# Kernel tuning notes

Hardware: AMD Instinct MI355X
Metric: run time of the kernel (lower is better)

## Reference

```python
import jax, jax.numpy as jnp
import numpy as np

N = 30000   # fluid particles
E = 480000  # edges
F = 4       # fluidFeatures (in channels)
P = 8       # RBF basis size per dim (dims=[8], 1D)
LAYERS = [32, 64, 64, 2]


def hat_basis(x, n):
    # 'linear' RBF: hat functions on n evenly spaced centers in [-1, 1]
    centers = jnp.linspace(-1.0, 1.0, n, dtype=x.dtype)
    spacing = 2.0 / (n - 1)
    return jnp.maximum(0.0, 1.0 - jnp.abs(x[:, None] - centers[None, :]) / spacing)  # [E, n]


def rbf_conv(x, fi, fj, d, W, b, mask, n_nodes):
    # x: [N, Cin]; d: [E, 1] clamped; W: [P, Cin, Cout]; b: [Cout]
    phi = hat_basis(d[:, 0], W.shape[0])      # [E, P]
    xj = x[fj]                                 # gather source features [E, Cin]
    msg = jnp.zeros((xj.shape[0], W.shape[2]), dtype=x.dtype)
    for p in range(W.shape[0]):                # small fixed P=8 loop keeps memory O(E*Cout)
        msg = msg + phi[:, p, None] * (xj @ W[p])
    msg = jnp.where(mask[:, None], msg, 0.0)   # centerIgnore: drop self edges fi==fj
    out = jax.ops.segment_sum(msg, fi, num_segments=n_nodes)  # scatter-reduce to targets
    return out + b


def _xavier(key, shape_in, shape_out):
    lim = float(np.sqrt(6.0 / (shape_in + shape_out)))
    return jax.random.uniform(key, (shape_in, shape_out), jnp.float32, -lim, lim)


def setup_inputs() -> dict:
    key = jax.random.key(0)
    ks = jax.random.split(key, 16)
    fluidFeatures = jax.random.normal(ks[0], (N, F), jnp.float32)
    fi = jax.random.randint(ks[1], (E,), 0, N)
    fj = jax.random.randint(ks[2], (E,), 0, N)
    distances = jax.random.normal(ks[3], (E, 1), jnp.float32)
    # conv channels: 4->32, 64->64, 64->64, 64->2
    cio = [(F, 32), (2 * 32, 64), (64, 64), (64, 2)]
    inp = {"fluidFeatures": fluidFeatures, "fi": fi, "fj": fj, "distances": distances}
    for li, (ci, co) in enumerate(cio):
        inp[f"cW{li}"] = jax.random.normal(ks[4 + li], (P, ci, co), jnp.float32) * (1.0 / np.sqrt(P * ci))
        inp[f"cb{li}"] = jnp.zeros((co,), jnp.float32)
        inp[f"fW{li}"] = _xavier(ks[8 + li], ci, co)   # stored [in, out]
        inp[f"fb{li}"] = jnp.zeros((co,), jnp.float32)
    return inp


def reference(fluidFeatures, fi, fj, distances,
              cW0, cb0, fW0, fb0, cW1, cb1, fW1, fb1,
              cW2, cb2, fW2, fb2, cW3, cb3, fW3, fb3):
    n_nodes = fluidFeatures.shape[0]
    mask = fi != fj                     # centerIgnore (mask instead of filter: jit-safe)
    d = jnp.clip(distances, -1.0, 1.0)

    conv0 = rbf_conv(fluidFeatures, fi, fj, d, cW0, cb0, mask, n_nodes)  # [N, 32]
    lin0 = fluidFeatures @ fW0 + fb0                                      # [N, 32]
    ans = jnp.concatenate([lin0, conv0], axis=1)                          # [N, 64]

    # i = 1: features[0]=32 != features[1]=64 -> no residual
    ansc = jax.nn.relu(ans)
    ans = rbf_conv(ansc, fi, fj, d, cW1, cb1, mask, n_nodes) + (ansc @ fW1 + fb1)
    # i = 2: features[1]==features[2]==64 and shapes match -> residual
    ansc = jax.nn.relu(ans)
    ans = rbf_conv(ansc, fi, fj, d, cW2, cb2, mask, n_nodes) + (ansc @ fW2 + fb2) + ans
    # i = 3: 64 -> 2, no residual
    ansc = jax.nn.relu(ans)
    ans = rbf_conv(ansc, fi, fj, d, cW3, cb3, mask, n_nodes) + (ansc @ fW3 + fb3)

    return ans  # dim == 1 (dims=[8]) -> no /128
```

## Files before the change

kernel.cpp:

```cpp
#include <hip/hip_runtime.h>


#define CAP 48

typedef __attribute__((ext_vector_type(8))) short short8;
typedef __attribute__((ext_vector_type(4))) short short4v;
typedef __attribute__((ext_vector_type(4))) float f32x4;

__device__ __forceinline__ short bf16s(float f) {
  unsigned u = __float_as_uint(f);
  return (short)((u + 0x7FFF + ((u >> 16) & 1)) >> 16);
}
__device__ __forceinline__ float b2f(unsigned short s) {
  return __uint_as_float(((unsigned)s) << 16);
}

__global__ void fill_prep(const float* __restrict__ dist,
                          const int* __restrict__ fi, const int* __restrict__ fj,
                          int* __restrict__ cnt, int* __restrict__ jw, int nE,
                          const float* __restrict__ cW1, const float* __restrict__ fW1,
                          const float* __restrict__ cW2, const float* __restrict__ fW2,
                          short* __restrict__ wt1, short* __restrict__ wt2,
                          int fillBlocks) {
  if ((int)blockIdx.x < fillBlocks) {
    int e = blockIdx.x * blockDim.x + threadIdx.x;
    if (e >= nE) return;
    int i = fi[e], j = fj[e];
    if (i == j) return;
    float d = fminf(1.0f, fmaxf(-1.0f, dist[e]));
    float u = (d + 1.0f) * 3.5f;
    int p = min((int)u, 6);
    float w0 = 1.0f - (u - (float)p);
    int wq = (int)(w0 * 16383.0f + 0.5f);
    int pos = atomicAdd(&cnt[i], 1);
    if (pos < CAP)
      jw[(size_t)i * CAP + pos] = j | (p << 15) | (wq << 18);
  } else {
    int idx = ((int)blockIdx.x - fillBlocks) * blockDim.x + threadIdx.x;
    if (idx >= 2 * 576 * 64) return;
    int sel = idx / (576 * 64);
    int r = idx - sel * (576 * 64);
    int col = r >> 6, ch = r & 63;
    const float* cW = sel ? cW2 : cW1;
    const float* fW = sel ? fW2 : fW1;
    float v;
    if (col < 512) {
      int p = col >> 6, co = col & 63;
      v = cW[((size_t)p * 64 + ch) * 64 + co];
    } else {
      v = fW[(size_t)ch * 64 + (col - 512)];
    }
    (sel ? wt2 : wt1)[(size_t)col * 64 + ch] = bf16s(v);
  }
}

__global__ __launch_bounds__(1024) void layer0_gemm(
    const float* __restrict__ X,
    const int* __restrict__ cnt, const int* __restrict__ jw,
    const float* __restrict__ cW0,
    const float* __restrict__ cb0,
    const float* __restrict__ fW0,
    const float* __restrict__ fb0,
    const short* __restrict__ WTul,
    unsigned short* __restrict__ UL, int n) {
  __shared__ float sW[1024];
  __shared__ float sF[128];
  __shared__ float sB[64];
  __shared__ float sacc[16][32];
  __shared__ __align__(16) unsigned short sXa[16 * 64];
  __shared__ __align__(16) short sUL[16 * 584];
  const int tid = threadIdx.x;
  const int w = tid >> 6;
  const int lane = tid & 63;
  const int nodeBase = blockIdx.x * 16;
  const int i = nodeBase + w;
  const bool valid = (i < n);

  sW[tid] = cW0[tid];
  if (tid < 128) sF[tid] = fW0[tid];
  else if (tid < 160) sB[tid - 128] = cb0[tid - 128];
  else if (tid < 192) sB[tid - 160 + 32] = fb0[tid - 160];
  if (tid < 512) sacc[tid >> 5][tid & 31] = 0.0f;
  __syncthreads();

  if (valid && lane < min(cnt[i], CAP)) {
    int v = jw[(size_t)i * CAP + lane];
    int j = v & 0x7FFF;
    int p = (v >> 15) & 7;
    float w0 = (float)((unsigned)v >> 18) * (1.0f / 16383.0f);
    float w1 = 1.0f - w0;
    float4 x = *(const float4*)(X + (size_t)j * 4);
    float* a = sacc[w];
    atomicAdd(&a[p * 4 + 0], w0 * x.x);
    atomicAdd(&a[p * 4 + 1], w0 * x.y);
    atomicAdd(&a[p * 4 + 2], w0 * x.z);
    atomicAdd(&a[p * 4 + 3], w0 * x.w);
    atomicAdd(&a[(p + 1) * 4 + 0], w1 * x.x);
    atomicAdd(&a[(p + 1) * 4 + 1], w1 * x.y);
    atomicAdd(&a[(p + 1) * 4 + 2], w1 * x.z);
    atomicAdd(&a[(p + 1) * 4 + 3], w1 * x.w);
  }
  __syncthreads();

  float vO = 0.0f;
  if (valid) {
    const float4 xi = *(const float4*)(X + (size_t)i * 4);
    if (lane < 32) {
      vO = sB[32 + lane];
      vO = fmaf(xi.x, sF[0 * 32 + lane], vO);
      vO = fmaf(xi.y, sF[1 * 32 + lane], vO);
      vO = fmaf(xi.z, sF[2 * 32 + lane], vO);
      vO = fmaf(xi.w, sF[3 * 32 + lane], vO);
    } else {
      const int cc = lane - 32;
      vO = sB[cc];
      #pragma unroll
      for (int k = 0; k < 32; ++k)
        vO = fmaf(sacc[w][k], sW[k * 32 + cc], vO);
    }
    vO = fmaxf(vO, 0.0f);
  }
  sXa[w * 64 + lane] = (unsigned short)bf16s(vO);
  __syncthreads();

  const int mrow = lane & 15;
  const int quad = lane >> 4;
  short8 b0 = *(const short8*)(sXa + mrow * 64 + quad * 8);
  short8 b1 = *(const short8*)(sXa + mrow * 64 + quad * 8 + 32);
  for (int t = w; t < 36; t += 16) {
    const short* aBase = WTul + (size_t)(t * 16 + mrow) * 64 + quad * 8;
    short8 a0 = *(const short8*)(aBase);
    short8 a1 = *(const short8*)(aBase + 32);
    f32x4 acc = {0, 0, 0, 0};
    acc = __builtin_amdgcn_mfma_f32_16x16x32_bf16(a0, b0, acc, 0, 0, 0);
    acc = __builtin_amdgcn_mfma_f32_16x16x32_bf16(a1, b1, acc, 0, 0, 0);
    short4v pk;
    #pragma unroll
    for (int reg = 0; reg < 4; ++reg) pk[reg] = bf16s(acc[reg]);
    *(short4v*)(sUL + mrow * 584 + t * 16 + quad * 4) = pk;
  }
  __syncthreads();
  const int r = tid >> 6;
  const int c0 = tid & 63;
  if (nodeBase + r < n) {
    unsigned short* dst = UL + (size_t)(nodeBase + r) * 576;
    #pragma unroll
    for (int chunk = c0; chunk < 72; chunk += 64)
      *(short8*)(dst + chunk * 8) = *(const short8*)(sUL + r * 584 + chunk * 8);
  }
}

__global__ __launch_bounds__(256) void gemm_ul(
    const unsigned short* __restrict__ Xb,
    const short* __restrict__ WTul,
    unsigned short* __restrict__ UL, int n) {
  __shared__ short sUL[16 * 584];
  const int lane = threadIdx.x & 63;
  const int w = threadIdx.x >> 6;
  const int mrow = lane & 15;
  const int quad = lane >> 4;
  const int nodeBase = blockIdx.x * 16;
  const int bnode = min(nodeBase + mrow, n - 1);
  const unsigned short* bBase = Xb + (size_t)bnode * 64 + quad * 8;
  short8 b0 = *(const short8*)(bBase);
  short8 b1 = *(const short8*)(bBase + 32);
  #pragma unroll
  for (int t = 0; t < 9; ++t) {
    const int ct = w * 9 + t;
    const short* aBase = WTul + (size_t)(ct * 16 + mrow) * 64 + quad * 8;
    short8 a0 = *(const short8*)(aBase);
    short8 a1 = *(const short8*)(aBase + 32);
    f32x4 acc = {0, 0, 0, 0};
    acc = __builtin_amdgcn_mfma_f32_16x16x32_bf16(a0, b0, acc, 0, 0, 0);
    acc = __builtin_amdgcn_mfma_f32_16x16x32_bf16(a1, b1, acc, 0, 0, 0);
    short4v pk;
    #pragma unroll
    for (int reg = 0; reg < 4; ++reg) pk[reg] = bf16s(acc[reg]);
    *(short4v*)(sUL + mrow * 584 + ct * 16 + quad * 4) = pk;
  }
  __syncthreads();
  const int r = threadIdx.x >> 4;
  const int c0 = threadIdx.x & 15;
  if (nodeBase + r < n) {
    unsigned short* dst = UL + (size_t)(nodeBase + r) * 576;
    #pragma unroll
    for (int chunk = c0; chunk < 72; chunk += 16)
      *(short8*)(dst + chunk * 8) = *(const short8*)(sUL + r * 584 + chunk * 8);
  }
}

template <bool HAS_RES, bool STORE_ANS, bool COMPUTE_T>
__global__ __launch_bounds__(256) void conv_gather(
    const unsigned short* __restrict__ UL,
    const int* __restrict__ cnt, const int* __restrict__ jw,
    const float* __restrict__ cb, const float* __restrict__ fb,
    const float* __restrict__ resid,
    const float* __restrict__ cW3,
    float* __restrict__ T,
    float* __restrict__ outAns,
    unsigned short* __restrict__ outAnsc, int n) {
  const int lane = threadIdx.x & 63;
  const int half = lane >> 5;
  const int pl = lane & 31;
  const int i = (blockIdx.x * blockDim.x + threadIdx.x) >> 6;
  if (i >= n) return;
  int rec = jw[(size_t)i * CAP + (lane < CAP ? lane : 0)];
  const int m = min(cnt[i], CAP);
  const int mc = m - 1;
  const unsigned short* ULrow = UL + (size_t)i * 576;
  const unsigned Lraw = ((const unsigned*)(ULrow + 512))[pl];
  float rv0 = 0.0f, rv1 = 0.0f;
  if (HAS_RES) {
    float2 rv = *(const float2*)(resid + (size_t)i * 64 + 2 * pl);
    rv0 = rv.x; rv1 = rv.y;
  }
  float accLo = 0.0f, accHi = 0.0f;
  for (int q0 = 0; q0 < m; q0 += 16) {
    unsigned raw[16];
    float w0s[16];
    #pragma unroll
    for (int k = 0; k < 16; ++k) {
      int v = __builtin_amdgcn_readlane(rec, min(q0 + k, mc));
      int j = v & 0x7FFF;
      int p = (v >> 15) & 7;
      w0s[k] = (float)((unsigned)v >> 18) * (1.0f / 16383.0f);
      raw[k] = ((const unsigned*)(UL + (size_t)j * 576 + p * 64))[lane];
    }
    #pragma unroll
    for (int k = 0; k < 16; ++k) {
      bool ok = (q0 + k < m);
      float w = half ? (1.0f - w0s[k]) : w0s[k];
      w = ok ? w : 0.0f;
      accLo = fmaf(w, __uint_as_float(raw[k] << 16), accLo);
      accHi = fmaf(w, __uint_as_float(raw[k] & 0xFFFF0000u), accHi);
    }
  }
  accLo += __shfl_xor(accLo, 32, 64);
  accHi += __shfl_xor(accHi, 32, 64);
  if (half == 0) {
    const int c0i = 2 * pl, c1i = c0i + 1;
    float L0 = __uint_as_float(Lraw << 16);
    float L1 = __uint_as_float(Lraw & 0xFFFF0000u);
    float o0 = accLo + L0 + cb[c0i] + fb[c0i] + rv0;
    float o1 = accHi + L1 + cb[c1i] + fb[c1i] + rv1;
    if (STORE_ANS)
      *(float2*)(outAns + (size_t)i * 64 + c0i) = make_float2(o0, o1);
    unsigned short xb0 = (unsigned short)bf16s(fmaxf(o0, 0.0f));
    unsigned short xb1 = (unsigned short)bf16s(fmaxf(o1, 0.0f));
    ((unsigned*)(outAnsc + (size_t)i * 64))[pl] = (unsigned)xb0 | ((unsigned)xb1 << 16);
    if (COMPUTE_T) {
      float x0 = b2f(xb0), x1 = b2f(xb1);
      float c[16];
      #pragma unroll
      for (int t = 0; t < 16; ++t) {
        const float* wrow = cW3 + ((size_t)(t >> 1) * 64) * 2 + (t & 1);
        c[t] = x0 * wrow[c0i * 2] + x1 * wrow[c1i * 2];
      }
      #pragma unroll
      for (int off = 16; off > 0; off >>= 1) {
        #pragma unroll
        for (int t = 0; t < 16; ++t) c[t] += __shfl_xor(c[t], off, 64);
      }
      if (pl == 0) {
        float* tr = T + (size_t)i * 16;
        #pragma unroll
        for (int t = 0; t < 16; ++t) tr[t] = c[t];
      }
    }
  }
}

__global__ __launch_bounds__(256, 4) void layer3_kernel(
    const unsigned short* __restrict__ Xb,
    const float* __restrict__ T,
    const int* __restrict__ cnt, const int* __restrict__ jw,
    const float* __restrict__ cb3, const float* __restrict__ fb3,
    const float* __restrict__ fW3,
    float* __restrict__ out, int n) {
  const int lane = threadIdx.x & 63;
  const int i = (blockIdx.x * blockDim.x + threadIdx.x) >> 6;
  if (i >= n) return;
  const int m = min(cnt[i], CAP);
  float c0 = 0.0f, c1 = 0.0f;
  if (lane < m) {
    int v = jw[(size_t)i * CAP + lane];
    int j = min(v & 0x7FFF, n - 1);
    int p = (v >> 15) & 7;
    float w0 = (float)((unsigned)v >> 18) * (1.0f / 16383.0f);
    float w1 = 1.0f - w0;
    const float* tb = T + (size_t)j * 16 + p * 2;
    float2 ta = *(const float2*)(tb);
    float2 tc = *(const float2*)(tb + 2);
    c0 = w0 * ta.x + w1 * tc.x;
    c1 = w0 * ta.y + w1 * tc.y;
  }
  float xi = b2f(Xb[(size_t)i * 64 + lane]);
  float2 fw = *(const float2*)(fW3 + lane * 2);
  c0 = fmaf(xi, fw.x, c0);
  c1 = fmaf(xi, fw.y, c1);
  #pragma unroll
  for (int off = 32; off > 0; off >>= 1) {
    c0 += __shfl_xor(c0, off, 64);
    c1 += __shfl_xor(c1, off, 64);
  }
  if (lane == 0) {
    out[(size_t)i * 2 + 0] = c0 + cb3[0] + fb3[0];
    out[(size_t)i * 2 + 1] = c1 + cb3[1] + fb3[1];
  }
}

extern "C" void kernel_launch(void* const* d_in, const int* in_sizes, int n_in,
                              void* d_out, int out_size, void* d_ws, size_t ws_size,
                              hipStream_t stream) {
  const float* X    = (const float*)d_in[0];
  const int*   fi   = (const int*)d_in[1];
  const int*   fj   = (const int*)d_in[2];
  const float* dist = (const float*)d_in[3];
  const float* cW0 = (const float*)d_in[4];  const float* cb0 = (const float*)d_in[5];
  const float* fW0 = (const float*)d_in[6];  const float* fb0 = (const float*)d_in[7];
  const float* cW1 = (const float*)d_in[8];  const float* cb1 = (const float*)d_in[9];
  const float* fW1 = (const float*)d_in[10]; const float* fb1 = (const float*)d_in[11];
  const float* cW2 = (const float*)d_in[12]; const float* cb2 = (const float*)d_in[13];
  const float* fW2 = (const float*)d_in[14]; const float* fb2 = (const float*)d_in[15];
  const float* cW3 = (const float*)d_in[16]; const float* cb3 = (const float*)d_in[17];
  const float* fW3 = (const float*)d_in[18]; const float* fb3 = (const float*)d_in[19];
  float* out = (float*)d_out;

  const int n  = in_sizes[0] / 4;
  const int nE = in_sizes[1];

  unsigned short* UL    = (unsigned short*)d_ws;
  unsigned short* ansc2 = UL + (size_t)n * 576;
  unsigned short* ansc1 = ansc2 + (size_t)n * 64;
  float*          ans1  = (float*)(ansc1 + (size_t)n * 64);
  float* T     = ans1 + (size_t)n * 64;
  short* wtul1 = (short*)(T + (size_t)n * 16);
  short* wtul2 = wtul1 + 576 * 64;
  int*   jw    = (int*)(wtul2 + 576 * 64);
  int*   cnt   = jw + (size_t)n * CAP;

  hipMemsetAsync(cnt, 0, (size_t)n * sizeof(int), stream);
  const int fillBlocks = (nE + 255) / 256;
  const int prepBlocks = (2 * 576 * 64 + 255) / 256;
  fill_prep<<<fillBlocks + prepBlocks, 256, 0, stream>>>(
      dist, fi, fj, cnt, jw, nE, cW1, fW1, cW2, fW2, wtul1, wtul2, fillBlocks);

  layer0_gemm<<<(n + 15) / 16, 1024, 0, stream>>>(X, cnt, jw, cW0, cb0, fW0, fb0,
                                                  wtul1, UL, n);
  conv_gather<false, true, false><<<(n * 64 + 255) / 256, 256, 0, stream>>>(
      UL, cnt, jw, cb1, fb1, nullptr, nullptr, nullptr, ans1, ansc1, n);
  gemm_ul<<<(n + 15) / 16, 256, 0, stream>>>(ansc1, wtul2, UL, n);
  conv_gather<true, false, true><<<(n * 64 + 255) / 256, 256, 0, stream>>>(
      UL, cnt, jw, cb2, fb2, ans1, cW3, T, nullptr, ansc2, n);
  layer3_kernel<<<(n * 64 + 255) / 256, 256, 0, stream>>>(ansc2, T, cnt, jw,
                                                          cb3, fb3, fW3, out, n);
}
```

Measured before the change: 258.9 us.

## Precompute per-node layer-0 transforms and gather them instead of LDS atomics

```diff
diff --git a/kernel.cpp b/kernel.cpp
--- a/kernel.cpp
+++ b/kernel.cpp
@@ -21,7 +21,11 @@
                           const float* __restrict__ cW1, const float* __restrict__ fW1,
                           const float* __restrict__ cW2, const float* __restrict__ fW2,
                           short* __restrict__ wt1, short* __restrict__ wt2,
-                          int fillBlocks) {
+                          const float* __restrict__ X,
+                          const float* __restrict__ cW0,
+                          const float* __restrict__ fW0,
+                          unsigned short* __restrict__ U0, int n,
+                          int fillBlocks, int prepBlocks) {
   if ((int)blockIdx.x < fillBlocks) {
     int e = blockIdx.x * blockDim.x + threadIdx.x;
     if (e >= nE) return;
@@ -35,7 +39,7 @@
     int pos = atomicAdd(&cnt[i], 1);
     if (pos < CAP)
       jw[(size_t)i * CAP + pos] = j | (p << 15) | (wq << 18);
-  } else {
+  } else if ((int)blockIdx.x < fillBlocks + prepBlocks) {
     int idx = ((int)blockIdx.x - fillBlocks) * blockDim.x + threadIdx.x;
     if (idx >= 2 * 576 * 64) return;
     int sel = idx / (576 * 64);
@@ -51,76 +55,84 @@
       v = fW[(size_t)ch * 64 + (col - 512)];
     }
     (sel ? wt2 : wt1)[(size_t)col * 64 + ch] = bf16s(v);
+  } else {
+    int idx = ((int)blockIdx.x - fillBlocks - prepBlocks) * blockDim.x + threadIdx.x;
+    if (idx >= n * 288) return;
+    int i = idx / 288, c = idx - i * 288;
+    const float* x = X + (size_t)i * 4;
+    float s = 0.0f;
+    if (c < 256) {
+      int p = c >> 5, co = c & 31;
+      #pragma unroll
+      for (int k = 0; k < 4; ++k) s = fmaf(x[k], cW0[((size_t)p * 4 + k) * 32 + co], s);
+    } else {
+      int co = c - 256;
+      #pragma unroll
+      for (int k = 0; k < 4; ++k) s = fmaf(x[k], fW0[(size_t)k * 32 + co], s);
+    }
+    U0[(size_t)i * 288 + c] = (unsigned short)bf16s(s);
   }
 }
 
 __global__ __launch_bounds__(1024) void layer0_gemm(
-    const float* __restrict__ X,
+    const unsigned short* __restrict__ U0,
     const int* __restrict__ cnt, const int* __restrict__ jw,
-    const float* __restrict__ cW0,
-    const float* __restrict__ cb0,
-    const float* __restrict__ fW0,
-    const float* __restrict__ fb0,
+    const float* __restrict__ cb0, const float* __restrict__ fb0,
     const short* __restrict__ WTul,
     unsigned short* __restrict__ UL, int n) {
-  __shared__ float sW[1024];
-  __shared__ float sF[128];
-  __shared__ float sB[64];
-  __shared__ float sacc[16][32];
   __shared__ __align__(16) unsigned short sXa[16 * 64];
   __shared__ __align__(16) short sUL[16 * 584];
   const int tid = threadIdx.x;
   const int w = tid >> 6;
   const int lane = tid & 63;
+  const int grp = lane >> 5;
+  const int gl = lane & 31;
   const int nodeBase = blockIdx.x * 16;
   const int i = nodeBase + w;
   const bool valid = (i < n);
-
-  sW[tid] = cW0[tid];
-  if (tid < 128) sF[tid] = fW0[tid];
-  else if (tid < 160) sB[tid - 128] = cb0[tid - 128];
-  else if (tid < 192) sB[tid - 160 + 32] = fb0[tid - 160];
-  if (tid < 512) sacc[tid >> 5][tid & 31] = 0.0f;
-  __syncthreads();
-
-  if (valid && lane < min(cnt[i], CAP)) {
-    int v = jw[(size_t)i * CAP + lane];
-    int j = v & 0x7FFF;
-    int p = (v >> 15) & 7;
-    float w0 = (float)((unsigned)v >> 18) * (1.0f / 16383.0f);
-    float w1 = 1.0f - w0;
-    float4 x = *(const float4*)(X + (size_t)j * 4);
-    float* a = sacc[w];
-    atomicAdd(&a[p * 4 + 0], w0 * x.x);
-    atomicAdd(&a[p * 4 + 1], w0 * x.y);
-    atomicAdd(&a[p * 4 + 2], w0 * x.z);
-    atomicAdd(&a[p * 4 + 3], w0 * x.w);
-    atomicAdd(&a[(p + 1) * 4 + 0], w1 * x.x);
-    atomicAdd(&a[(p + 1) * 4 + 1], w1 * x.y);
-    atomicAdd(&a[(p + 1) * 4 + 2], w1 * x.z);
-    atomicAdd(&a[(p + 1) * 4 + 3], w1 * x.w);
-  }
-  __syncthreads();
-
-  float vO = 0.0f;
-  if (valid) {
-    const float4 xi = *(const float4*)(X + (size_t)i * 4);
-    if (lane < 32) {
-      vO = sB[32 + lane];
-      vO = fmaf(xi.x, sF[0 * 32 + lane], vO);
-      vO = fmaf(xi.y, sF[1 * 32 + lane], vO);
-      vO = fmaf(xi.z, sF[2 * 32 + lane], vO);
-      vO = fmaf(xi.w, sF[3 * 32 + lane], vO);
-    } else {
-      const int cc = lane - 32;
-      vO = sB[cc];
-      #pragma unroll
-      for (int k = 0; k < 32; ++k)
-        vO = fmaf(sacc[w][k], sW[k * 32 + cc], vO);
-    }
-    vO = fmaxf(vO, 0.0f);
-  }
-  sXa[w * 64 + lane] = (unsigned short)bf16s(vO);
+  const int ic = valid ? i : 0;
+
+  int rec = jw[(size_t)ic * CAP + (lane < CAP ? lane : 0)];
+  const int m = valid ? min(cnt[ic], CAP) : 0;
+  const int mc = m - 1;
+  float accLo = 0.0f, accHi = 0.0f;
+  for (int q0 = 0; q0 < m; q0 += 16) {
+    unsigned raw[8];
+    float ws[8];
+    #pragma unroll
+    for (int k = 0; k < 8; ++k) {
+      int eA = q0 + 2 * k;
+      int vA = __builtin_amdgcn_readlane(rec, min(eA, mc));
+      int vB = __builtin_amdgcn_readlane(rec, min(eA + 1, mc));
+      int v = grp ? vB : vA;
+      int j = v & 0x7FFF;
+      int p = (v >> 15) & 7;
+      float w0 = (float)((unsigned)v >> 18) * (1.0f / 16383.0f);
+      float wgt = (gl < 16) ? w0 : (1.0f - w0);
+      ws[k] = (eA + grp < m) ? wgt : 0.0f;
+      raw[k] = ((const unsigned*)(U0 + (size_t)j * 288 + p * 32))[gl];
+    }
+    #pragma unroll
+    for (int k = 0; k < 8; ++k) {
+      accLo = fmaf(ws[k], __uint_as_float(raw[k] << 16), accLo);
+      accHi = fmaf(ws[k], __uint_as_float(raw[k] & 0xFFFF0000u), accHi);
+    }
+  }
+  accLo += __shfl_xor(accLo, 16, 64);
+  accHi += __shfl_xor(accHi, 16, 64);
+  accLo += __shfl_xor(accLo, 32, 64);
+  accHi += __shfl_xor(accHi, 32, 64);
+  if (lane < 16) {
+    const int l = lane;
+    float c0v = fmaxf(accLo + cb0[2 * l], 0.0f);
+    float c1v = fmaxf(accHi + cb0[2 * l + 1], 0.0f);
+    unsigned lr = ((const unsigned*)(U0 + (size_t)ic * 288 + 256))[l];
+    float l0 = fmaxf(__uint_as_float(lr << 16) + fb0[2 * l], 0.0f);
+    float l1 = fmaxf(__uint_as_float(lr & 0xFFFF0000u) + fb0[2 * l + 1], 0.0f);
+    unsigned* row = (unsigned*)(sXa + w * 64);
+    row[l] = (unsigned)(unsigned short)bf16s(l0) | ((unsigned)(unsigned short)bf16s(l1) << 16);
+    row[16 + l] = (unsigned)(unsigned short)bf16s(c0v) | ((unsigned)(unsigned short)bf16s(c1v) << 16);
+  }
   __syncthreads();
 
   const int mrow = lane & 15;
@@ -338,14 +350,17 @@
   short* wtul2 = wtul1 + 576 * 64;
   int*   jw    = (int*)(wtul2 + 576 * 64);
   int*   cnt   = jw + (size_t)n * CAP;
+  unsigned short* U0 = (unsigned short*)(cnt + n);
 
   hipMemsetAsync(cnt, 0, (size_t)n * sizeof(int), stream);
   const int fillBlocks = (nE + 255) / 256;
   const int prepBlocks = (2 * 576 * 64 + 255) / 256;
-  fill_prep<<<fillBlocks + prepBlocks, 256, 0, stream>>>(
-      dist, fi, fj, cnt, jw, nE, cW1, fW1, cW2, fW2, wtul1, wtul2, fillBlocks);
-
-  layer0_gemm<<<(n + 15) / 16, 1024, 0, stream>>>(X, cnt, jw, cW0, cb0, fW0, fb0,
+  const int u0Blocks   = (n * 288 + 255) / 256;
+  fill_prep<<<fillBlocks + prepBlocks + u0Blocks, 256, 0, stream>>>(
+      dist, fi, fj, cnt, jw, nE, cW1, fW1, cW2, fW2, wtul1, wtul2,
+      X, cW0, fW0, U0, n, fillBlocks, prepBlocks);
+
+  layer0_gemm<<<(n + 15) / 16, 1024, 0, stream>>>(U0, cnt, jw, cb0, fb0,
                                                   wtul1, UL, n);
   conv_gather<false, true, false><<<(n * 64 + 255) / 256, 256, 0, stream>>>(
       UL, cnt, jw, cb1, fb1, nullptr, nullptr, nullptr, ans1, ansc1, n);
```

After: 261.2 us. No clear change (+0.9%).
